# Kernel tuning notes

Measured on AMD Instinct MI355X. Metric: run time of the kernel, lower is better.

The kernel has to match this reference:

```python
import jax, jax.numpy as jnp
import numpy as np

D_MODEL = 1024
D_HIDDEN = 32   # per-head MPS bond dimension
N_HEADS = 8
D_FF = 4096
EPS_LN = 1e-5
EPS_NORM = 1e-6


def layernorm(x, g, b):
    m = jnp.mean(x, axis=-1, keepdims=True)
    v = jnp.mean(jnp.square(x - m), axis=-1, keepdims=True)
    return (x - m) * jax.lax.rsqrt(v + EPS_LN) * g + b


def mps_recurrence(x, Wa, ba, h0, Wo, bo):
    # x: [B,S,D]. Per-token per-head transfer matrices A_t in R^{dh x dh}.
    B, S, D = x.shape
    A = (x @ Wa + ba).reshape(B, S, N_HEADS, D_HIDDEN, D_HIDDEN)
    A = jnp.moveaxis(A, 1, 0)  # [S,B,H,dh,dh]
    h_init = jnp.broadcast_to(h0, (B, N_HEADS, D_HIDDEN))  # [B,H,dh]

    def step(h, A_t):
        h = jnp.einsum('bhij,bhj->bhi', A_t, h)
        h = h / (jnp.linalg.norm(h, axis=-1, keepdims=True) + EPS_NORM)
        return h, h

    _, ys = jax.lax.scan(step, h_init, A)          # ys: [S,B,H,dh]
    ys = jnp.moveaxis(ys, 0, 1).reshape(B, S, N_HEADS * D_HIDDEN)
    return ys @ Wo + bo                            # [B,S,D]


def setup_inputs() -> dict:
    key = jax.random.key(0)
    ks = jax.random.split(key, 12)
    B, S, D = 4, 2048, D_MODEL
    inv = 1.0 / np.sqrt(D)
    inv_hd = 1.0 / np.sqrt(N_HEADS * D_HIDDEN)
    return {
        'x': jax.random.normal(ks[0], (B, S, D), jnp.float32),
        'ln1_g': jnp.ones((D,), jnp.float32),
        'ln1_b': jnp.zeros((D,), jnp.float32),
        'Wa': jax.random.normal(ks[1], (D, N_HEADS * D_HIDDEN * D_HIDDEN), jnp.float32) * inv,
        'ba': jnp.zeros((N_HEADS * D_HIDDEN * D_HIDDEN,), jnp.float32),
        'h0': jax.random.normal(ks[2], (N_HEADS, D_HIDDEN), jnp.float32) / np.sqrt(D_HIDDEN),
        'Wo': jax.random.normal(ks[3], (N_HEADS * D_HIDDEN, D), jnp.float32) * inv_hd,
        'bo': jnp.zeros((D,), jnp.float32),
        'ln2_g': jnp.ones((D,), jnp.float32),
        'ln2_b': jnp.zeros((D,), jnp.float32),
        'W1': jax.random.normal(ks[4], (D, D_FF), jnp.float32) * inv,
        'b1': jnp.zeros((D_FF,), jnp.float32),
        'W2': jax.random.normal(ks[5], (D_FF, D), jnp.float32) / np.sqrt(D_FF),
        'b2': jnp.zeros((D,), jnp.float32),
    }


def reference(x, ln1_g, ln1_b, Wa, ba, h0, Wo, bo, ln2_g, ln2_b, W1, b1, W2, b2):
    # Dropout in eval mode (identity).
    x = x + mps_recurrence(layernorm(x, ln1_g, ln1_b), Wa, ba, h0, Wo, bo)
    h = layernorm(x, ln2_g, ln2_b)
    ffn = jax.nn.gelu(h @ W1 + b1, approximate=False) @ W2 + b2
    return x + ffn
```

## Files before the change

kernel.cpp:

```cpp
#include <hip/hip_runtime.h>
#include <hip/hip_bf16.h>
#include <math.h>

typedef float f32x4 __attribute__((ext_vector_type(4)));
typedef __bf16 bf16x4 __attribute__((ext_vector_type(4)));
typedef __bf16 bf16x8 __attribute__((ext_vector_type(8)));

#define AS1(p) ((const __attribute__((address_space(1))) void*)(p))
#define AS3(p) ((__attribute__((address_space(3))) void*)(p))

static constexpr int D_MODEL = 1024;
static constexpr int S_LEN   = 2048;
static constexpr int BATCH   = 4;
static constexpr int NTOK    = BATCH * S_LEN;
static constexpr int NH      = 8;
static constexpr int DH      = 32;
static constexpr int NA      = NH * DH * DH;
static constexpr int D_FF    = 4096;
static constexpr int CHUNK   = 16;
static constexpr int NCHUNK  = S_LEN / CHUNK;

__device__ __forceinline__ void xcd_swizzle(int& bx, int& by) {
  int gx = gridDim.x;
  int orig = by * gx + bx;
  int r8 = orig & 7, j = orig >> 3;
  int bxn = j % gx, grp = j / gx;
  bx = bxn;
  by = grp * 8 + r8;
}

__device__ __forceinline__ float gelu_erf_fast(float v) {
  float z = fabsf(v) * 0.70710678118654752f;
  float t = __builtin_amdgcn_rcpf(fmaf(0.3275911f, z, 1.0f));
  float p = t * (0.254829592f + t * (-0.284496736f + t * (1.421413741f +
            t * (-1.453152027f + t * 1.061405429f))));
  float e = __builtin_amdgcn_exp2f(-1.4426950408889634f * z * z);
  float er = 1.0f - p * e;
  er = (v < 0.0f) ? -er : er;
  return 0.5f * v * (1.0f + er);
}

__global__ __launch_bounds__(256) void transpose_bf16(
    const float* __restrict__ in, __bf16* __restrict__ out, int R, int C) {
  __shared__ float tile[32][33];
  int tx = threadIdx.x & 31, ty = threadIdx.x >> 5;
  int c0 = blockIdx.x * 32, r0 = blockIdx.y * 32;
  for (int i = ty; i < 32; i += 8)
    tile[i][tx] = in[(size_t)(r0 + i) * C + c0 + tx];
  __syncthreads();
  for (int i = ty; i < 32; i += 8)
    out[(size_t)(c0 + i) * R + r0 + tx] = (__bf16)tile[tx][i];
}

__global__ __launch_bounds__(256) void transpose_split(
    const float* __restrict__ in, __bf16* __restrict__ ohi,
    __bf16* __restrict__ olo, int R, int C) {
  __shared__ float tile[32][33];
  int tx = threadIdx.x & 31, ty = threadIdx.x >> 5;
  int c0 = blockIdx.x * 32, r0 = blockIdx.y * 32;
  for (int i = ty; i < 32; i += 8)
    tile[i][tx] = in[(size_t)(r0 + i) * C + c0 + tx];
  __syncthreads();
  for (int i = ty; i < 32; i += 8) {
    float v = tile[tx][i];
    __bf16 h = (__bf16)v;
    ohi[(size_t)(c0 + i) * R + r0 + tx] = h;
    olo[(size_t)(c0 + i) * R + r0 + tx] = (__bf16)(v - (float)h);
  }
}

template <int MODE>
__global__ __launch_bounds__(256) void ln_kernel(
    const float* __restrict__ in, const float* __restrict__ g,
    const float* __restrict__ bta, void* __restrict__ outv,
    void* __restrict__ outv2) {
  int row = blockIdx.x, tid = threadIdx.x;
  const float4* in4 = (const float4*)(in + (size_t)row * D_MODEL);
  float4 v = in4[tid];
  float s  = v.x + v.y + v.z + v.w;
  float ss = v.x * v.x + v.y * v.y + v.z * v.z + v.w * v.w;
  for (int o = 32; o; o >>= 1) { s += __shfl_down(s, o); ss += __shfl_down(ss, o); }
  __shared__ float ps[4], pq[4];
  int lane = tid & 63, w = tid >> 6;
  if (lane == 0) { ps[w] = s; pq[w] = ss; }
  __syncthreads();
  s  = ps[0] + ps[1] + ps[2] + ps[3];
  ss = pq[0] + pq[1] + pq[2] + pq[3];
  float mean = s * (1.0f / D_MODEL);
  float var  = ss * (1.0f / D_MODEL) - mean * mean;
  float inv  = rsqrtf(fmaxf(var, 0.0f) + 1e-5f);
  float4 gv = ((const float4*)g)[tid];
  float4 bv = ((const float4*)bta)[tid];
  float o0 = (v.x - mean) * inv * gv.x + bv.x;
  float o1 = (v.y - mean) * inv * gv.y + bv.y;
  float o2 = (v.z - mean) * inv * gv.z + bv.z;
  float o3 = (v.w - mean) * inv * gv.w + bv.w;
  if (MODE == 1) {
    float4 o = {o0, o1, o2, o3};
    ((float4*)outv)[(size_t)row * (D_MODEL / 4) + tid] = o;
  } else if (MODE == 0) {
    bf16x4 o;
    o[0] = (__bf16)o0; o[1] = (__bf16)o1; o[2] = (__bf16)o2; o[3] = (__bf16)o3;
    ((bf16x4*)outv)[(size_t)row * (D_MODEL / 4) + tid] = o;
  } else {
    bf16x4 oh, ol;
    oh[0] = (__bf16)o0; oh[1] = (__bf16)o1; oh[2] = (__bf16)o2; oh[3] = (__bf16)o3;
    ol[0] = (__bf16)(o0 - (float)oh[0]);
    ol[1] = (__bf16)(o1 - (float)oh[1]);
    ol[2] = (__bf16)(o2 - (float)oh[2]);
    ol[3] = (__bf16)(o3 - (float)oh[3]);
    ((bf16x4*)outv )[(size_t)row * (D_MODEL / 4) + tid] = oh;
    ((bf16x4*)outv2)[(size_t)row * (D_MODEL / 4) + tid] = ol;
  }
}

__global__ __launch_bounds__(256) void gemm_split_f32out(
    const __bf16* __restrict__ Ahi, const __bf16* __restrict__ Alo,
    const __bf16* __restrict__ BThi, const __bf16* __restrict__ BTlo,
    const float* __restrict__ bias, float* __restrict__ out,
    int M, int N, int K) {
  __shared__ __bf16 Ash[128 * 32], Asl[128 * 32];
  __shared__ __bf16 Bsh[128 * 32], Bsl[128 * 32];
  const int tid = threadIdx.x;
  const int lane = tid & 63, w = tid >> 6;
  int bx = blockIdx.x, by = blockIdx.y;
  xcd_swizzle(bx, by);
  const int m0 = by * 128, n0 = bx * 128;
  const int wm = (w >> 1) * 64, wn = (w & 1) * 64;

  f32x4 acc[4][4];
#pragma unroll
  for (int a = 0; a < 4; a++)
#pragma unroll
    for (int b = 0; b < 4; b++)
#pragma unroll
      for (int r = 0; r < 4; r++) acc[a][b][r] = 0.0f;

  const int srow = tid >> 2;
  const int soff = (tid & 3) * 16;
  const size_t goff0 = (size_t)(m0 + srow) * K + (soff >> 1);
  const size_t goff1 = (size_t)(m0 + srow + 64) * K + (soff >> 1);
  const size_t hoff0 = (size_t)(n0 + srow) * K + (soff >> 1);
  const size_t hoff1 = (size_t)(n0 + srow + 64) * K + (soff >> 1);
  const int l0 = srow * 64 + soff, l1 = (srow + 64) * 64 + soff;

  const int fm = lane & 15, fq = lane >> 4;
  for (int k0 = 0; k0 < K; k0 += 32) {
    __builtin_amdgcn_global_load_lds(AS1(Ahi + goff0 + k0), AS3((char*)Ash + l0), 16, 0, 0);
    __builtin_amdgcn_global_load_lds(AS1(Ahi + goff1 + k0), AS3((char*)Ash + l1), 16, 0, 0);
    __builtin_amdgcn_global_load_lds(AS1(Alo + goff0 + k0), AS3((char*)Asl + l0), 16, 0, 0);
    __builtin_amdgcn_global_load_lds(AS1(Alo + goff1 + k0), AS3((char*)Asl + l1), 16, 0, 0);
    __builtin_amdgcn_global_load_lds(AS1(BThi + hoff0 + k0), AS3((char*)Bsh + l0), 16, 0, 0);
    __builtin_amdgcn_global_load_lds(AS1(BThi + hoff1 + k0), AS3((char*)Bsh + l1), 16, 0, 0);
    __builtin_amdgcn_global_load_lds(AS1(BTlo + hoff0 + k0), AS3((char*)Bsl + l0), 16, 0, 0);
    __builtin_amdgcn_global_load_lds(AS1(BTlo + hoff1 + k0), AS3((char*)Bsl + l1), 16, 0, 0);
    __syncthreads();
    bf16x8 ah[4], al[4], bh[4], bl[4];
#pragma unroll
    for (int t = 0; t < 4; t++) {
      int o = (wm + t * 16 + fm) * 64 + fq * 16;
      ah[t] = *(const bf16x8*)((const char*)Ash + o);
      al[t] = *(const bf16x8*)((const char*)Asl + o);
    }
#pragma unroll
    for (int t = 0; t < 4; t++) {
      int o = (wn + t * 16 + fm) * 64 + fq * 16;
      bh[t] = *(const bf16x8*)((const char*)Bsh + o);
      bl[t] = *(const bf16x8*)((const char*)Bsl + o);
    }
#pragma unroll
    for (int tm = 0; tm < 4; tm++)
#pragma unroll
      for (int tn = 0; tn < 4; tn++) {
        acc[tm][tn] = __builtin_amdgcn_mfma_f32_16x16x32_bf16(ah[tm], bh[tn], acc[tm][tn], 0, 0, 0);
        acc[tm][tn] = __builtin_amdgcn_mfma_f32_16x16x32_bf16(ah[tm], bl[tn], acc[tm][tn], 0, 0, 0);
        acc[tm][tn] = __builtin_amdgcn_mfma_f32_16x16x32_bf16(al[tm], bh[tn], acc[tm][tn], 0, 0, 0);
      }
    __syncthreads();
  }

#pragma unroll
  for (int tn = 0; tn < 4; tn++) {
    int col = n0 + wn + tn * 16 + fm;
    float bv = bias[col];
#pragma unroll
    for (int tm = 0; tm < 4; tm++) {
#pragma unroll
      for (int r = 0; r < 4; r++) {
        int row = m0 + wm + tm * 16 + fq * 4 + r;
        out[(size_t)row * N + col] = acc[tm][tn][r] + bv;
      }
    }
  }
}

enum { EPI_BF16_BIAS = 0, EPI_BF16_BIAS_GELU = 1, EPI_F32_BIAS_RES = 2 };

template <int EPI>
__global__ __launch_bounds__(256) void gemm_bf16(
    const __bf16* __restrict__ Amat, const __bf16* __restrict__ BT,
    const float* __restrict__ bias, const float* __restrict__ res,
    void* __restrict__ out, int M, int N, int K) {
  __shared__ __bf16 smem[2 * 128 * 32];
  __bf16* As = smem;
  __bf16* Bs = smem + 128 * 32;
  const int tid = threadIdx.x;
  const int lane = tid & 63, w = tid >> 6;
  int bx = blockIdx.x, by = blockIdx.y;
  xcd_swizzle(bx, by);
  const int m0 = by * 128, n0 = bx * 128;
  const int wm = (w >> 1) * 64, wn = (w & 1) * 64;

  f32x4 acc[4][4];
#pragma unroll
  for (int a = 0; a < 4; a++)
#pragma unroll
    for (int b = 0; b < 4; b++)
#pragma unroll
      for (int r = 0; r < 4; r++) acc[a][b][r] = 0.0f;

  const int srow = tid >> 2;
  const int soff = (tid & 3) * 16;
  const __bf16* gA0 = Amat + (size_t)(m0 + srow) * K + (soff >> 1);
  const __bf16* gA1 = Amat + (size_t)(m0 + srow + 64) * K + (soff >> 1);
  const __bf16* gB0 = BT + (size_t)(n0 + srow) * K + (soff >> 1);
  const __bf16* gB1 = BT + (size_t)(n0 + srow + 64) * K + (soff >> 1);
  char* lA0 = (char*)As + srow * 64 + soff;
  char* lA1 = (char*)As + (srow + 64) * 64 + soff;
  char* lB0 = (char*)Bs + srow * 64 + soff;
  char* lB1 = (char*)Bs + (srow + 64) * 64 + soff;

  const int fm = lane & 15, fq = lane >> 4;
  for (int k0 = 0; k0 < K; k0 += 32) {
    __builtin_amdgcn_global_load_lds(AS1(gA0 + k0), AS3(lA0), 16, 0, 0);
    __builtin_amdgcn_global_load_lds(AS1(gA1 + k0), AS3(lA1), 16, 0, 0);
    __builtin_amdgcn_global_load_lds(AS1(gB0 + k0), AS3(lB0), 16, 0, 0);
    __builtin_amdgcn_global_load_lds(AS1(gB1 + k0), AS3(lB1), 16, 0, 0);
    __syncthreads();
    bf16x8 af[4], bf[4];
#pragma unroll
    for (int t = 0; t < 4; t++)
      af[t] = *(const bf16x8*)((const char*)As + (wm + t * 16 + fm) * 64 + fq * 16);
#pragma unroll
    for (int t = 0; t < 4; t++)
      bf[t] = *(const bf16x8*)((const char*)Bs + (wn + t * 16 + fm) * 64 + fq * 16);
#pragma unroll
    for (int tm = 0; tm < 4; tm++)
#pragma unroll
      for (int tn = 0; tn < 4; tn++)
        acc[tm][tn] = __builtin_amdgcn_mfma_f32_16x16x32_bf16(af[tm], bf[tn], acc[tm][tn], 0, 0, 0);
    __syncthreads();
  }

  if (EPI == EPI_BF16_BIAS_GELU) {
    float bvs[4];
#pragma unroll
    for (int tn = 0; tn < 4; tn++) bvs[tn] = bias[n0 + wn + tn * 16 + fm];
    char* patch = (char*)smem + w * 4096;
#pragma unroll
    for (int h2 = 0; h2 < 2; h2++) {
#pragma unroll
      for (int tmi = 0; tmi < 2; tmi++) {
        int tm = h2 * 2 + tmi;
#pragma unroll
        for (int tn = 0; tn < 4; tn++)
#pragma unroll
          for (int r = 0; r < 4; r++) {
            float vv = gelu_erf_fast(acc[tm][tn][r] + bvs[tn]);
            *(__bf16*)(patch + (tmi * 16 + fq * 4 + r) * 128 + (tn * 16 + fm) * 2) =
                (__bf16)vv;
          }
      }
      asm volatile("s_waitcnt lgkmcnt(0)" ::: "memory");
      int lrow = lane >> 3, lcb = (lane & 7) * 16;
#pragma unroll
      for (int rr = 0; rr < 4; rr++) {
        bf16x8 ov = *(const bf16x8*)(patch + (rr * 8 + lrow) * 128 + lcb);
        size_t grow = (size_t)(m0 + wm + h2 * 32 + rr * 8 + lrow);
        *(bf16x8*)((__bf16*)out + grow * N + n0 + wn + (lane & 7) * 8) = ov;
      }
      if (h2 == 0) asm volatile("s_waitcnt lgkmcnt(0)" ::: "memory");
    }
  } else {
#pragma unroll
    for (int tn = 0; tn < 4; tn++) {
      int col = n0 + wn + tn * 16 + fm;
      float bv = bias[col];
#pragma unroll
      for (int tm = 0; tm < 4; tm++) {
#pragma unroll
        for (int r = 0; r < 4; r++) {
          int row = m0 + wm + tm * 16 + fq * 4 + r;
          float v = acc[tm][tn][r] + bv;
          size_t idx = (size_t)row * N + col;
          if (EPI == EPI_F32_BIAS_RES) {
            ((float*)out)[idx] = v + res[idx];
          } else {
            ((__bf16*)out)[idx] = (__bf16)v;
          }
        }
      }
    }
  }
}

__global__ __launch_bounds__(64) void mps_chunkprod_f32(
    float* __restrict__ A) {
  int bid = blockIdx.x;
  int c = bid & 127, hh = bid >> 7;
  int lane = threadIdx.x;
  int jj = lane & 31, half = lane >> 5;
  __shared__ float Albuf[2][DH * DH];

  float curc[32];
#pragma unroll
  for (int k = 0; k < 32; k++) curc[k] = (k == jj) ? 1.0f : 0.0f;

  float* Abase = A + (size_t)(c * CHUNK) * NA + (size_t)hh * (DH * DH);

  {
    const float4* src = (const float4*)Abase;
    float4* dst = (float4*)Albuf[0];
#pragma unroll
    for (int r = 0; r < 4; r++) dst[lane + 64 * r] = src[lane + 64 * r];
  }
  __syncthreads();

  for (int t = 0; t < CHUNK; t++) {
    int cb = t & 1;
    float4 pf[4];
    if (t + 1 < CHUNK) {
      const float4* srcn = (const float4*)(Abase + (size_t)(t + 1) * NA);
#pragma unroll
      for (int r = 0; r < 4; r++) pf[r] = srcn[lane + 64 * r];
    }
    float nxt[16];
#pragma unroll
    for (int i16 = 0; i16 < 16; i16++) {
      const float4* ap = (const float4*)&Albuf[cb][(half * 16 + i16) * 32];
      float a0 = 0.f, a1 = 0.f, a2 = 0.f, a3 = 0.f;
#pragma unroll
      for (int k4 = 0; k4 < 8; k4++) {
        float4 av = ap[k4];
        a0 += av.x * curc[k4 * 4 + 0];
        a1 += av.y * curc[k4 * 4 + 1];
        a2 += av.z * curc[k4 * 4 + 2];
        a3 += av.w * curc[k4 * 4 + 3];
      }
      nxt[i16] = (a0 + a1) + (a2 + a3);
    }
    {
      float* slot = Abase + (size_t)t * NA;
#pragma unroll
      for (int i16 = 0; i16 < 16; i16++)
        slot[(half * 16 + i16) * 32 + jj] = nxt[i16];
    }
#pragma unroll
    for (int i16 = 0; i16 < 16; i16++) {
      float mine  = nxt[i16];
      float other = __shfl_xor(mine, 32);
      curc[i16]      = (half == 0) ? mine  : other;
      curc[16 + i16] = (half == 0) ? other : mine;
    }
    if (t + 1 < CHUNK) {
      float4* dst = (float4*)Albuf[cb ^ 1];
#pragma unroll
      for (int r = 0; r < 4; r++) dst[lane + 64 * r] = pf[r];
      __syncthreads();
    }
  }
}

__global__ __launch_bounds__(64) void mps_chunkscan(
    const float* __restrict__ pref, const float* __restrict__ h0,
    float* __restrict__ hstart) {
  int hh = blockIdx.x;
  int lane = threadIdx.x, i = lane & 31, half = lane >> 5;
  float hv = h0[hh * 32 + i];
  const size_t cstride = (size_t)CHUNK * NA;
  const float* row = pref + (size_t)(CHUNK - 1) * NA + (size_t)hh * (DH * DH)
                     + i * 32 + half * 16;
  int kb = half * 16;

  float4 pf0[4], pf1[4];
#pragma unroll
  for (int r = 0; r < 4; r++) pf0[r] = ((const float4*)row)[r];
#pragma unroll
  for (int r = 0; r < 4; r++) pf1[r] = ((const float4*)(row + cstride))[r];

  for (int c = 0; c < NCHUNK; c++) {
    if (lane < 32) hstart[((size_t)hh * NCHUNK + c) * 32 + i] = hv;
    float4 cur[4];
#pragma unroll
    for (int r = 0; r < 4; r++) cur[r] = pf0[r];
#pragma unroll
    for (int r = 0; r < 4; r++) pf0[r] = pf1[r];
    int cn = (c + 2 < NCHUNK) ? (c + 2) : (NCHUNK - 1);
#pragma unroll
    for (int r = 0; r < 4; r++)
      pf1[r] = ((const float4*)(row + (size_t)cn * cstride))[r];

    float a0 = 0.f, a1 = 0.f, a2 = 0.f, a3 = 0.f;
#pragma unroll
    for (int j4 = 0; j4 < 4; j4++) {
      float4 pv = cur[j4];
      a0 += pv.x * __shfl(hv, kb + j4 * 4 + 0);
      a1 += pv.y * __shfl(hv, kb + j4 * 4 + 1);
      a2 += pv.z * __shfl(hv, kb + j4 * 4 + 2);
      a3 += pv.w * __shfl(hv, kb + j4 * 4 + 3);
    }
    float y = (a0 + a1) + (a2 + a3);
    y += __shfl_xor(y, 32);
    float nn = y * y;
#pragma unroll
    for (int o = 16; o; o >>= 1) nn += __shfl_xor(nn, o);
    hv = y / (sqrtf(nn) + 1e-6f);
  }
}

__global__ __launch_bounds__(256) void mps_expand_par(
    const float* __restrict__ pref, const float* __restrict__ hstart,
    __bf16* __restrict__ ys, int tok0base) {
  int w = threadIdx.x >> 6, lane = threadIdx.x & 63;
  int i = lane & 31, half = lane >> 5;
  int task = blockIdx.x * 4 + w;
  int hh = task & 7, tok = task >> 3;
  int c = tok >> 4;
  int kb = half * 16;

  float hv = hstart[((size_t)hh * NCHUNK + c) * 32 + i];
  const float4* Mr = (const float4*)(pref + (size_t)tok * NA
                     + (size_t)hh * (DH * DH) + i * 32 + half * 16);
  float4 m0 = Mr[0], m1 = Mr[1], m2 = Mr[2], m3 = Mr[3];

  float a0 = 0.f, a1 = 0.f, a2 = 0.f, a3 = 0.f;
  a0 += m0.x * __shfl(hv, kb + 0);  a1 += m0.y * __shfl(hv, kb + 1);
  a2 += m0.z * __shfl(hv, kb + 2);  a3 += m0.w * __shfl(hv, kb + 3);
  a0 += m1.x * __shfl(hv, kb + 4);  a1 += m1.y * __shfl(hv, kb + 5);
  a2 += m1.z * __shfl(hv, kb + 6);  a3 += m1.w * __shfl(hv, kb + 7);
  a0 += m2.x * __shfl(hv, kb + 8);  a1 += m2.y * __shfl(hv, kb + 9);
  a2 += m2.z * __shfl(hv, kb + 10); a3 += m2.w * __shfl(hv, kb + 11);
  a0 += m3.x * __shfl(hv, kb + 12); a1 += m3.y * __shfl(hv, kb + 13);
  a2 += m3.z * __shfl(hv, kb + 14); a3 += m3.w * __shfl(hv, kb + 15);
  float y = (a0 + a1) + (a2 + a3);
  y += __shfl_xor(y, 32);
  float nn = y * y;
#pragma unroll
  for (int o = 16; o; o >>= 1) nn += __shfl_xor(nn, o);
  float hvo = y / (sqrtf(nn) + 1e-6f);
  if (lane < 32)
    ys[(size_t)(tok0base + tok) * (NH * DH) + hh * 32 + i] = (__bf16)hvo;
}

extern "C" void kernel_launch(void* const* d_in, const int* in_sizes, int n_in,
                              void* d_out, int out_size, void* d_ws, size_t ws_size,
                              hipStream_t stream) {
  const float* x     = (const float*)d_in[0];
  const float* ln1_g = (const float*)d_in[1];
  const float* ln1_b = (const float*)d_in[2];
  const float* Wa    = (const float*)d_in[3];
  const float* ba    = (const float*)d_in[4];
  const float* h0    = (const float*)d_in[5];
  const float* Wo    = (const float*)d_in[6];
  const float* bo    = (const float*)d_in[7];
  const float* ln2_g = (const float*)d_in[8];
  const float* ln2_b = (const float*)d_in[9];
  const float* W1    = (const float*)d_in[10];
  const float* b1    = (const float*)d_in[11];
  const float* W2    = (const float*)d_in[12];
  const float* b2    = (const float*)d_in[13];
  float* out = (float*)d_out;

  char* wsb = (char*)d_ws;
  size_t off = 0;
  auto alloc = [&](size_t bytes) -> void* {
    void* p = wsb + off;
    off += (bytes + 255) & ~(size_t)255;
    return p;
  };
  __bf16* WoT   = (__bf16*)alloc((size_t)(NH * DH) * D_MODEL * 2);
  __bf16* W1T   = (__bf16*)alloc((size_t)D_MODEL * D_FF * 2);
  __bf16* W2T   = (__bf16*)alloc((size_t)D_FF * D_MODEL * 2);
  __bf16* ys    = (__bf16*)alloc((size_t)NTOK * NH * DH * 2);
  float*  hst   = (float*) alloc((size_t)NH * NCHUNK * DH * 4);
  __bf16* xnh   = (__bf16*)alloc((size_t)NTOK * D_MODEL * 2);
  __bf16* xnl   = (__bf16*)alloc((size_t)NTOK * D_MODEL * 2);
  __bf16* WaTh  = (__bf16*)alloc((size_t)D_MODEL * NA * 2);
  __bf16* WaTl  = (__bf16*)alloc((size_t)D_MODEL * NA * 2);
  size_t tail0 = off;
  float*  Af32 = (float*) alloc((size_t)S_LEN * NA * 4);
  __bf16* mid  = (__bf16*)(wsb + tail0);

  transpose_bf16<<<dim3(D_MODEL / 32, (NH * DH) / 32), 256, 0, stream>>>(Wo, WoT, NH * DH, D_MODEL);
  transpose_bf16<<<dim3(D_FF / 32, D_MODEL / 32), 256, 0, stream>>>(W1, W1T, D_MODEL, D_FF);
  transpose_bf16<<<dim3(D_MODEL / 32, D_FF / 32), 256, 0, stream>>>(W2, W2T, D_FF, D_MODEL);
  transpose_split<<<dim3(NA / 32, D_MODEL / 32), 256, 0, stream>>>(Wa, WaTh, WaTl, D_MODEL, NA);

  ln_kernel<2><<<NTOK, 256, 0, stream>>>(x, ln1_g, ln1_b, xnh, xnl);

  for (int b = 0; b < BATCH; b++) {
    gemm_split_f32out<<<dim3(NA / 128, S_LEN / 128), 256, 0, stream>>>(
        xnh + (size_t)b * S_LEN * D_MODEL, xnl + (size_t)b * S_LEN * D_MODEL,
        WaTh, WaTl, ba, Af32, S_LEN, NA, D_MODEL);
    mps_chunkprod_f32<<<NH * NCHUNK, 64, 0, stream>>>(Af32);
    mps_chunkscan<<<NH, 64, 0, stream>>>(Af32, h0, hst);
    mps_expand_par<<<(S_LEN * NH) / 4, 256, 0, stream>>>(Af32, hst, ys, b * S_LEN);
  }

  gemm_bf16<EPI_F32_BIAS_RES><<<dim3(D_MODEL / 128, NTOK / 128), 256, 0, stream>>>(
      ys, WoT, bo, x, out, NTOK, D_MODEL, NH * DH);

  ln_kernel<0><<<NTOK, 256, 0, stream>>>(out, ln2_g, ln2_b, xnh, nullptr);

  gemm_bf16<EPI_BF16_BIAS_GELU><<<dim3(D_FF / 128, NTOK / 128), 256, 0, stream>>>(
      xnh, W1T, b1, nullptr, mid, NTOK, D_FF, D_MODEL);

  gemm_bf16<EPI_F32_BIAS_RES><<<dim3(D_MODEL / 128, NTOK / 128), 256, 0, stream>>>(
      mid, W2T, b2, out, out, NTOK, D_MODEL, D_FF);
}
```

Measured before the change: 1.515 ms.

## Replace Wa projection and FFN-up GEMMs with 256x256 pipelined 8-wave kernel

Adds a gemm8 kernel using 256x256 tiles, 512 threads, K=64 steps, XOR-swizzled LDS, and double-buffered global_load_lds prefetch interleaved with MFMA phases under setprio and sched barriers. The split-precision Wa GEMM is reformulated as three K=1024 passes (hi*hi, hi*lo, lo*hi) concatenated into a K-loop of 48 tiles, rather than three MFMAs per fragment. The W1+GELU GEMM also moves to this kernel. This aims at more data reuse per LDS load and better overlap of memory and compute, at the cost of 128KB LDS per block and fewer, larger blocks, which may leave CUs underused.

```diff
diff --git a/kernel.cpp b/kernel.cpp
--- a/kernel.cpp
+++ b/kernel.cpp
@@ -114,87 +114,174 @@
   }
 }
 
-__global__ __launch_bounds__(256) void gemm_split_f32out(
-    const __bf16* __restrict__ Ahi, const __bf16* __restrict__ Alo,
-    const __bf16* __restrict__ BThi, const __bf16* __restrict__ BTlo,
-    const float* __restrict__ bias, float* __restrict__ out,
+enum { EPI_BF16_BIAS = 0, EPI_BF16_BIAS_GELU = 1, EPI_F32_BIAS_RES = 2,
+       EPI_F32_BIAS_ONLY = 3 };
+
+#define PH_SYNC()                                      \
+  do {                                                 \
+    __builtin_amdgcn_sched_barrier(0);                 \
+    __builtin_amdgcn_s_barrier();                      \
+    __builtin_amdgcn_sched_barrier(0);                 \
+  } while (0)
+#define LGKM0()                                        \
+  do {                                                 \
+    asm volatile("s_waitcnt lgkmcnt(0)" ::: "memory"); \
+    __builtin_amdgcn_sched_barrier(0);                 \
+  } while (0)
+#define GEMM8_QUAD(I0, J0)                                                   \
+  do {                                                                       \
+    __builtin_amdgcn_s_setprio(1);                                           \
+    _Pragma("unroll") for (int i_ = 0; i_ < 4; ++i_)                         \
+    _Pragma("unroll") for (int j_ = 0; j_ < 2; ++j_)                         \
+    _Pragma("unroll") for (int k_ = 0; k_ < 2; ++k_)                         \
+      acc[(I0) + i_][(J0) + j_] = __builtin_amdgcn_mfma_f32_16x16x32_bf16(   \
+          a[(I0) + i_][k_], b[(J0) + j_][k_], acc[(I0) + i_][(J0) + j_],     \
+          0, 0, 0);                                                          \
+    __builtin_amdgcn_s_setprio(0);                                           \
+  } while (0)
+
+template <int SPLIT, int EPI>
+__global__ __launch_bounds__(512, 2) void gemm8(
+    const __bf16* __restrict__ pA, const __bf16* __restrict__ pA2,
+    const __bf16* __restrict__ pB, const __bf16* __restrict__ pB2,
+    const float* __restrict__ bias, void* __restrict__ out,
     int M, int N, int K) {
-  __shared__ __bf16 Ash[128 * 32], Asl[128 * 32];
-  __shared__ __bf16 Bsh[128 * 32], Bsl[128 * 32];
+  __shared__ alignas(16) char lds[131072];
   const int tid = threadIdx.x;
   const int lane = tid & 63, w = tid >> 6;
+  const int fm = lane & 15, fq = lane >> 4;
+  const int wm2 = w >> 2, wn4 = w & 3;
   int bx = blockIdx.x, by = blockIdx.y;
   xcd_swizzle(bx, by);
-  const int m0 = by * 128, n0 = bx * 128;
-  const int wm = (w >> 1) * 64, wn = (w & 1) * 64;
-
-  f32x4 acc[4][4];
-#pragma unroll
-  for (int a = 0; a < 4; a++)
-#pragma unroll
-    for (int b = 0; b < 4; b++)
-#pragma unroll
-      for (int r = 0; r < 4; r++) acc[a][b][r] = 0.0f;
-
-  const int srow = tid >> 2;
-  const int soff = (tid & 3) * 16;
-  const size_t goff0 = (size_t)(m0 + srow) * K + (soff >> 1);
-  const size_t goff1 = (size_t)(m0 + srow + 64) * K + (soff >> 1);
-  const size_t hoff0 = (size_t)(n0 + srow) * K + (soff >> 1);
-  const size_t hoff1 = (size_t)(n0 + srow + 64) * K + (soff >> 1);
-  const int l0 = srow * 64 + soff, l1 = (srow + 64) * 64 + soff;
-
-  const int fm = lane & 15, fq = lane >> 4;
-  for (int k0 = 0; k0 < K; k0 += 32) {
-    __builtin_amdgcn_global_load_lds(AS1(Ahi + goff0 + k0), AS3((char*)Ash + l0), 16, 0, 0);
-    __builtin_amdgcn_global_load_lds(AS1(Ahi + goff1 + k0), AS3((char*)Ash + l1), 16, 0, 0);
-    __builtin_amdgcn_global_load_lds(AS1(Alo + goff0 + k0), AS3((char*)Asl + l0), 16, 0, 0);
-    __builtin_amdgcn_global_load_lds(AS1(Alo + goff1 + k0), AS3((char*)Asl + l1), 16, 0, 0);
-    __builtin_amdgcn_global_load_lds(AS1(BThi + hoff0 + k0), AS3((char*)Bsh + l0), 16, 0, 0);
-    __builtin_amdgcn_global_load_lds(AS1(BThi + hoff1 + k0), AS3((char*)Bsh + l1), 16, 0, 0);
-    __builtin_amdgcn_global_load_lds(AS1(BTlo + hoff0 + k0), AS3((char*)Bsl + l0), 16, 0, 0);
-    __builtin_amdgcn_global_load_lds(AS1(BTlo + hoff1 + k0), AS3((char*)Bsl + l1), 16, 0, 0);
-    __syncthreads();
-    bf16x8 ah[4], al[4], bh[4], bl[4];
-#pragma unroll
-    for (int t = 0; t < 4; t++) {
-      int o = (wm + t * 16 + fm) * 64 + fq * 16;
-      ah[t] = *(const bf16x8*)((const char*)Ash + o);
-      al[t] = *(const bf16x8*)((const char*)Asl + o);
-    }
-#pragma unroll
-    for (int t = 0; t < 4; t++) {
-      int o = (wn + t * 16 + fm) * 64 + fq * 16;
-      bh[t] = *(const bf16x8*)((const char*)Bsh + o);
-      bl[t] = *(const bf16x8*)((const char*)Bsl + o);
-    }
-#pragma unroll
-    for (int tm = 0; tm < 4; tm++)
-#pragma unroll
-      for (int tn = 0; tn < 4; tn++) {
-        acc[tm][tn] = __builtin_amdgcn_mfma_f32_16x16x32_bf16(ah[tm], bh[tn], acc[tm][tn], 0, 0, 0);
-        acc[tm][tn] = __builtin_amdgcn_mfma_f32_16x16x32_bf16(ah[tm], bl[tn], acc[tm][tn], 0, 0, 0);
-        acc[tm][tn] = __builtin_amdgcn_mfma_f32_16x16x32_bf16(al[tm], bh[tn], acc[tm][tn], 0, 0, 0);
-      }
-    __syncthreads();
-  }
-
-#pragma unroll
-  for (int tn = 0; tn < 4; tn++) {
-    int col = n0 + wn + tn * 16 + fm;
-    float bv = bias[col];
-#pragma unroll
-    for (int tm = 0; tm < 4; tm++) {
-#pragma unroll
-      for (int r = 0; r < 4; r++) {
-        int row = m0 + wm + tm * 16 + fq * 4 + r;
-        out[(size_t)row * N + col] = acc[tm][tn][r] + bv;
-      }
-    }
-  }
-}
-
-enum { EPI_BF16_BIAS = 0, EPI_BF16_BIAS_GELU = 1, EPI_F32_BIAS_RES = 2 };
+  const int m0 = by * 256, n0 = bx * 256;
+  const int NT = SPLIT ? 48 : (K >> 6);
+  const int KS = SPLIT ? D_MODEL : K;
+
+  const int lrow8 = lane >> 3;
+  const int lslot = ((lane & 7) ^ lrow8) << 3;
+
+  auto stageA = [&](int kt, int h) {
+    const __bf16* base = SPLIT ? ((kt < 32) ? pA : pA2) : pA;
+    int kc = SPLIT ? ((kt & 15) << 6) : (kt << 6);
+    char* d0 = lds + ((kt & 1) << 15);
+#pragma unroll
+    for (int j = 0; j < 2; ++j) {
+      int rb = h * 128 + j * 64 + w * 8;
+      const __bf16* src = base + (size_t)(m0 + rb + lrow8) * KS + kc + lslot;
+      __builtin_amdgcn_global_load_lds(AS1(src), AS3(d0 + rb * 128 + lane * 16), 16, 0, 0);
+    }
+  };
+  auto stageB = [&](int kt, int h) {
+    const __bf16* base = SPLIT ? ((kt >= 16 && kt < 32) ? pB2 : pB) : pB;
+    int kc = SPLIT ? ((kt & 15) << 6) : (kt << 6);
+    char* d0 = lds + 65536 + ((kt & 1) << 15);
+#pragma unroll
+    for (int j = 0; j < 2; ++j) {
+      int rb = h * 128 + j * 64 + w * 8;
+      const __bf16* src = base + (size_t)(n0 + rb + lrow8) * KS + kc + lslot;
+      __builtin_amdgcn_global_load_lds(AS1(src), AS3(d0 + rb * 128 + lane * 16), 16, 0, 0);
+    }
+  };
+  auto rdA = [&](int bo, int i, int ks) -> bf16x8 {
+    int row = wm2 * 128 + i * 16 + fm;
+    return *(const bf16x8*)(lds + bo + row * 128 +
+                            ((((ks << 2) + fq) ^ (row & 7)) << 4));
+  };
+  auto rdB = [&](int bo, int j, int ks) -> bf16x8 {
+    int row = wn4 * 64 + j * 16 + fm;
+    return *(const bf16x8*)(lds + 65536 + bo + row * 128 +
+                            ((((ks << 2) + fq) ^ (row & 7)) << 4));
+  };
+
+  f32x4 acc[8][4];
+#pragma unroll
+  for (int i = 0; i < 8; ++i)
+#pragma unroll
+    for (int j = 0; j < 4; ++j)
+#pragma unroll
+      for (int r = 0; r < 4; ++r) acc[i][j][r] = 0.0f;
+
+  stageA(0, 0); stageA(0, 1); stageB(0, 0); stageB(0, 1);
+  if (NT > 1) { stageA(1, 0); stageA(1, 1); }
+  __builtin_amdgcn_sched_barrier(0);
+  if (NT > 1) asm volatile("s_waitcnt vmcnt(4)" ::: "memory");
+  else        asm volatile("s_waitcnt vmcnt(0)" ::: "memory");
+  PH_SYNC();
+
+  for (int t = 0; t < NT; ++t) {
+    const int bo = (t & 1) << 15;
+    bf16x8 a[8][2], b[4][2];
+#pragma unroll
+    for (int i = 0; i < 4; ++i) { a[i][0] = rdA(bo, i, 0); a[i][1] = rdA(bo, i, 1); }
+#pragma unroll
+    for (int j = 0; j < 2; ++j) { b[j][0] = rdB(bo, j, 0); b[j][1] = rdB(bo, j, 1); }
+    if (t + 1 < NT) stageB(t + 1, 0);
+    PH_SYNC();
+    LGKM0();
+    GEMM8_QUAD(0, 0);
+    PH_SYNC();
+#pragma unroll
+    for (int j = 2; j < 4; ++j) { b[j][0] = rdB(bo, j, 0); b[j][1] = rdB(bo, j, 1); }
+    if (t + 1 < NT) stageB(t + 1, 1);
+    PH_SYNC();
+    LGKM0();
+    GEMM8_QUAD(0, 2);
+    PH_SYNC();
+#pragma unroll
+    for (int i = 4; i < 8; ++i) { a[i][0] = rdA(bo, i, 0); a[i][1] = rdA(bo, i, 1); }
+    PH_SYNC();
+    LGKM0();
+    GEMM8_QUAD(4, 0);
+    PH_SYNC();
+    if (t + 2 < NT) { stageA(t + 2, 0); stageA(t + 2, 1); }
+    PH_SYNC();
+    GEMM8_QUAD(4, 2);
+    __builtin_amdgcn_sched_barrier(0);
+    if (t + 2 < NT)
+      asm volatile("s_waitcnt vmcnt(4)" ::: "memory");
+    else if (t + 1 < NT)
+      asm volatile("s_waitcnt vmcnt(0)" ::: "memory");
+    PH_SYNC();
+  }
+
+  if (EPI == EPI_F32_BIAS_ONLY) {
+    float* outF = (float*)out;
+#pragma unroll
+    for (int j = 0; j < 4; ++j) {
+      int col = n0 + wn4 * 64 + j * 16 + fm;
+      float bv = bias[col];
+#pragma unroll
+      for (int i = 0; i < 8; ++i)
+#pragma unroll
+        for (int r = 0; r < 4; ++r) {
+          int row = m0 + wm2 * 128 + i * 16 + fq * 4 + r;
+          outF[(size_t)row * N + col] = acc[i][j][r] + bv;
+        }
+    }
+  } else {
+    char* patch = lds + w * 16384;
+    float bv4[4];
+#pragma unroll
+    for (int j = 0; j < 4; ++j) bv4[j] = bias[n0 + wn4 * 64 + j * 16 + fm];
+#pragma unroll
+    for (int i = 0; i < 8; ++i)
+#pragma unroll
+      for (int j = 0; j < 4; ++j)
+#pragma unroll
+        for (int r = 0; r < 4; ++r) {
+          float v = gelu_erf_fast(acc[i][j][r] + bv4[j]);
+          *(__bf16*)(patch + (i * 16 + fq * 4 + r) * 128 + (j * 16 + fm) * 2) =
+              (__bf16)v;
+        }
+    asm volatile("s_waitcnt lgkmcnt(0)" ::: "memory");
+#pragma unroll
+    for (int rr = 0; rr < 16; ++rr) {
+      bf16x8 ov = *(const bf16x8*)(patch + (rr * 8 + lrow8) * 128 + (lane & 7) * 16);
+      size_t grow = (size_t)(m0 + wm2 * 128 + rr * 8 + lrow8);
+      *(bf16x8*)((__bf16*)out + grow * N + n0 + wn4 * 64 + (lane & 7) * 8) = ov;
+    }
+  }
+}
 
 template <int EPI>
 __global__ __launch_bounds__(256) void gemm_bf16(
@@ -252,52 +339,24 @@
     __syncthreads();
   }
 
-  if (EPI == EPI_BF16_BIAS_GELU) {
-    float bvs[4];
-#pragma unroll
-    for (int tn = 0; tn < 4; tn++) bvs[tn] = bias[n0 + wn + tn * 16 + fm];
-    char* patch = (char*)smem + w * 4096;
-#pragma unroll
-    for (int h2 = 0; h2 < 2; h2++) {
-#pragma unroll
-      for (int tmi = 0; tmi < 2; tmi++) {
-        int tm = h2 * 2 + tmi;
-#pragma unroll
-        for (int tn = 0; tn < 4; tn++)
-#pragma unroll
-          for (int r = 0; r < 4; r++) {
-            float vv = gelu_erf_fast(acc[tm][tn][r] + bvs[tn]);
-            *(__bf16*)(patch + (tmi * 16 + fq * 4 + r) * 128 + (tn * 16 + fm) * 2) =
-                (__bf16)vv;
-          }
-      }
-      asm volatile("s_waitcnt lgkmcnt(0)" ::: "memory");
-      int lrow = lane >> 3, lcb = (lane & 7) * 16;
-#pragma unroll
-      for (int rr = 0; rr < 4; rr++) {
-        bf16x8 ov = *(const bf16x8*)(patch + (rr * 8 + lrow) * 128 + lcb);
-        size_t grow = (size_t)(m0 + wm + h2 * 32 + rr * 8 + lrow);
-        *(bf16x8*)((__bf16*)out + grow * N + n0 + wn + (lane & 7) * 8) = ov;
-      }
-      if (h2 == 0) asm volatile("s_waitcnt lgkmcnt(0)" ::: "memory");
-    }
-  } else {
-#pragma unroll
-    for (int tn = 0; tn < 4; tn++) {
-      int col = n0 + wn + tn * 16 + fm;
-      float bv = bias[col];
-#pragma unroll
-      for (int tm = 0; tm < 4; tm++) {
-#pragma unroll
-        for (int r = 0; r < 4; r++) {
-          int row = m0 + wm + tm * 16 + fq * 4 + r;
-          float v = acc[tm][tn][r] + bv;
-          size_t idx = (size_t)row * N + col;
-          if (EPI == EPI_F32_BIAS_RES) {
-            ((float*)out)[idx] = v + res[idx];
-          } else {
-            ((__bf16*)out)[idx] = (__bf16)v;
-          }
+#pragma unroll
+  for (int tn = 0; tn < 4; tn++) {
+    int col = n0 + wn + tn * 16 + fm;
+    float bv = bias[col];
+#pragma unroll
+    for (int tm = 0; tm < 4; tm++) {
+#pragma unroll
+      for (int r = 0; r < 4; r++) {
+        int row = m0 + wm + tm * 16 + fq * 4 + r;
+        float v = acc[tm][tn][r] + bv;
+        size_t idx = (size_t)row * N + col;
+        if (EPI == EPI_F32_BIAS_RES) {
+          ((float*)out)[idx] = v + res[idx];
+        } else if (EPI == EPI_BF16_BIAS_GELU) {
+          v = gelu_erf_fast(v);
+          ((__bf16*)out)[idx] = (__bf16)v;
+        } else {
+          ((__bf16*)out)[idx] = (__bf16)v;
         }
       }
     }
@@ -499,7 +558,7 @@
   ln_kernel<2><<<NTOK, 256, 0, stream>>>(x, ln1_g, ln1_b, xnh, xnl);
 
   for (int b = 0; b < BATCH; b++) {
-    gemm_split_f32out<<<dim3(NA / 128, S_LEN / 128), 256, 0, stream>>>(
+    gemm8<1, EPI_F32_BIAS_ONLY><<<dim3(NA / 256, S_LEN / 256), 512, 0, stream>>>(
         xnh + (size_t)b * S_LEN * D_MODEL, xnl + (size_t)b * S_LEN * D_MODEL,
         WaTh, WaTl, ba, Af32, S_LEN, NA, D_MODEL);
     mps_chunkprod_f32<<<NH * NCHUNK, 64, 0, stream>>>(Af32);
@@ -512,8 +571,8 @@
 
   ln_kernel<0><<<NTOK, 256, 0, stream>>>(out, ln2_g, ln2_b, xnh, nullptr);
 
-  gemm_bf16<EPI_BF16_BIAS_GELU><<<dim3(D_FF / 128, NTOK / 128), 256, 0, stream>>>(
-      xnh, W1T, b1, nullptr, mid, NTOK, D_FF, D_MODEL);
+  gemm8<0, EPI_BF16_BIAS_GELU><<<dim3(D_FF / 256, NTOK / 256), 512, 0, stream>>>(
+      xnh, nullptr, W1T, nullptr, b1, mid, NTOK, D_FF, D_MODEL);
 
   gemm_bf16<EPI_F32_BIAS_RES><<<dim3(D_MODEL / 128, NTOK / 128), 256, 0, stream>>>(
       mid, W2T, b2, out, out, NTOK, D_MODEL, D_FF);
```

Result: faster. 1.473 ms (-2.7%).
